# Kernel tuning notes

Measured on AMD Instinct MI355X. Metric: run time of the kernel, lower is better.

## Reference

```python
import jax, jax.numpy as jnp
import numpy as np

PATCH = 9  # patch_size (search window 9x9, i.e. displacement radius 4)


def setup_inputs() -> dict:
    key = jax.random.key(0)
    k1, k2 = jax.random.split(key)
    input1 = jax.random.normal(k1, (8, 128, 96, 128), dtype=jnp.float32)
    input2 = jax.random.normal(k2, (8, 128, 96, 128), dtype=jnp.float32)
    return {"input1": input1, "input2": input2}


def _correlation(input1, input2):
    # kernel_size=1, stride=1, padding=0, dilation=1, dilation_patch=1
    b, c, h, w = input1.shape
    pad_lo = (PATCH - 1) // 2
    pad_hi = PATCH // 2
    p2 = jnp.pad(input2, ((0, 0), (0, 0), (pad_lo, pad_hi), (pad_lo, pad_hi)))

    offs = jnp.arange(PATCH)
    ii, jj = jnp.meshgrid(offs, offs, indexing="ij")
    shifts = jnp.stack([ii.ravel(), jj.ravel()], axis=-1)  # (PATCH*PATCH, 2)

    def one_shift(off):
        win = jax.lax.dynamic_slice(p2, (0, 0, off[0], off[1]), (b, c, h, w))
        # channel-wise dot product at every spatial location
        return jnp.einsum("bchw,bchw->bhw", input1, win)

    corr = jax.vmap(one_shift)(shifts)          # (PATCH*PATCH, b, h, w)
    corr = corr.reshape(PATCH, PATCH, b, h, w)
    return corr.transpose(2, 0, 1, 3, 4)        # (b, PATCH, PATCH, h, w)


def reference(input1, input2):
    return _correlation(input1, input2)
```

## Files before the change

### kernel.cpp

```cpp
#include <hip/hip_runtime.h>

#define HH 96
#define WW 128
#define PP 9
#define RAD 4
#define YT 2
#define CCH 8
#define NCHUNK 16
#define TDI 3
#define ROWS2 (YT + TDI - 1)
#define WB 64
#define HALO (WB + 2 * RAD)
#define GS2 73
#define GS1 65
#define NPAIR2 (ROWS2 * (HALO / 2))
#define NPAIR1 (YT * (WB / 2))
#define NT 192
#define CHS (HH * WW)
#define CSTEP (CCH * CHS)

typedef __fp16 h2v __attribute__((ext_vector_type(2)));
union HU { unsigned int u; h2v h; };

__device__ __forceinline__ unsigned int pk(float a, float b) {
    HU r; r.h = __builtin_amdgcn_cvt_pkrtz(a, b); return r.u;
}
__device__ __forceinline__ float dot2(unsigned int a, unsigned int b, float c) {
    HU ua, ub; ua.u = a; ub.u = b;
    return __builtin_amdgcn_fdot2(ua.h, ub.h, c, false);
}
__device__ __forceinline__ int swz(int g) { return g ^ ((g >> 3) & 7); }

__global__ __launch_bounds__(NT, 6)
void corr_kernel(const float* __restrict__ in1, const float* __restrict__ in2,
                 float* __restrict__ out)
{
    __shared__ uint4 s2[2][ROWS2 * GS2];
    __shared__ uint4 s1[2][YT * GS1];

    const int tid = threadIdx.x;
    const int by  = blockIdx.x >> 1;
    const int bx  = blockIdx.x & 1;
    const int y0  = by * YT;
    const int x0b = bx * WB;
    const int b   = blockIdx.y;
    const int dib = blockIdx.z * TDI;

    const int di3 = tid >> 6;
    const int yl  = (tid >> 5) & 1;
    const int xg  = tid & 31;
    const int x0l = 2 * xg;

    const float* b1 = in1 + (size_t)b * 128 * CHS;
    const float* b2 = in2 + (size_t)b * 128 * CHS;

    const float* tp0; int dA0, dB0; bool tv0, t0is2;
    if (tid < NPAIR2) {
        const int row = tid / 36;
        const int pp  = tid - row * 36;
        const int gy  = y0 - RAD + dib + row;
        const int gx  = x0b + 2 * pp - RAD;
        t0is2 = true;
        tv0   = ((unsigned)gy < HH) && ((unsigned)gx < WW);
        tp0   = b2 + (gy * WW + gx);
        dA0   = row * GS2 + swz(2 * pp);
        dB0   = row * GS2 + swz(2 * pp + 1);
    } else {
        const int u   = tid - NPAIR2;
        const int row = u >> 5;
        const int pp  = u & 31;
        t0is2 = false;
        tv0   = true;
        tp0   = b1 + ((y0 + row) * WW + x0b + 2 * pp);
        dA0   = row * GS1 + swz(2 * pp);
        dB0   = row * GS1 + swz(2 * pp + 1);
    }
    const bool act1 = (tid < 16);
    const float* tp1 = b1 + ((y0 + 1) * WW + x0b + 2 * (16 + tid));
    const int dA1 = GS1 + swz(2 * (16 + tid));
    const int dB1 = GS1 + swz(2 * (16 + tid) + 1);

    float acc[PP][2];
    #pragma unroll
    for (int j = 0; j < PP; ++j) { acc[j][0] = 0.f; acc[j][1] = 0.f; }

    for (int cc = 0; cc < NCHUNK; ++cc) {
        const int buf = cc & 1;
        const int co  = cc * CSTEP;

        {
            float2 f[8];
            #pragma unroll
            for (int j = 0; j < 8; ++j)
                f[j] = tv0 ? *reinterpret_cast<const float2*>(tp0 + co + j * CHS)
                           : make_float2(0.f, 0.f);
            uint4 gA, gB;
            gA.x = pk(f[0].x, f[1].x); gA.y = pk(f[2].x, f[3].x);
            gA.z = pk(f[4].x, f[5].x); gA.w = pk(f[6].x, f[7].x);
            gB.x = pk(f[0].y, f[1].y); gB.y = pk(f[2].y, f[3].y);
            gB.z = pk(f[4].y, f[5].y); gB.w = pk(f[6].y, f[7].y);
            if (t0is2) { s2[buf][dA0] = gA; s2[buf][dB0] = gB; }
            else       { s1[buf][dA0] = gA; s1[buf][dB0] = gB; }
        }
        if (act1) {
            float2 f[8];
            #pragma unroll
            for (int j = 0; j < 8; ++j)
                f[j] = *reinterpret_cast<const float2*>(tp1 + co + j * CHS);
            uint4 gA, gB;
            gA.x = pk(f[0].x, f[1].x); gA.y = pk(f[2].x, f[3].x);
            gA.z = pk(f[4].x, f[5].x); gA.w = pk(f[6].x, f[7].x);
            gB.x = pk(f[0].y, f[1].y); gB.y = pk(f[2].y, f[3].y);
            gB.z = pk(f[4].y, f[5].y); gB.w = pk(f[6].y, f[7].y);
            s1[buf][dA1] = gA; s1[buf][dB1] = gB;
        }
        __syncthreads();

        {
            const uint4* ar = &s1[buf][yl * GS1];
            const uint4 a0 = ar[swz(x0l)];
            const uint4 a1 = ar[swz(x0l + 1)];
            const uint4* r2 = &s2[buf][(yl + di3) * GS2];
            #pragma unroll
            for (int w = 0; w < PP + 1; ++w) {
                const uint4 v = r2[swz(x0l + w)];
                if (w <= PP - 1) {
                    float t = acc[w][0];
                    t = dot2(v.x, a0.x, t); t = dot2(v.y, a0.y, t);
                    t = dot2(v.z, a0.z, t); t = dot2(v.w, a0.w, t);
                    acc[w][0] = t;
                }
                if (w >= 1) {
                    float t = acc[w - 1][1];
                    t = dot2(v.x, a1.x, t); t = dot2(v.y, a1.y, t);
                    t = dot2(v.z, a1.z, t); t = dot2(v.w, a1.w, t);
                    acc[w - 1][1] = t;
                }
            }
        }
    }

    const int y  = y0 + yl;
    const int di = dib + di3;
    const int xo = x0b + x0l;
    #pragma unroll
    for (int dj = 0; dj < PP; ++dj) {
        float* op = out + ((((size_t)(b * PP + di)) * PP + dj) * HH + y) * WW + xo;
        *reinterpret_cast<float2*>(op) = make_float2(acc[dj][0], acc[dj][1]);
    }
}

extern "C" void kernel_launch(void* const* d_in, const int* in_sizes, int n_in,
                              void* d_out, int out_size, void* d_ws, size_t ws_size,
                              hipStream_t stream) {
    const float* in1 = (const float*)d_in[0];
    const float* in2 = (const float*)d_in[1];
    float* out = (float*)d_out;
    dim3 grid((HH / YT) * 2, 8, 3);
    dim3 block(NT);
    corr_kernel<<<grid, block, 0, stream>>>(in1, in2, out);
}
```

Measured before the change: 180.3 us.

## Cover all nine row displacements per block to share input tiles

Removes the grid z-split over row-displacement groups. Each block now has 576 threads and covers all 9 row displacements, so it stages a 10-row halo of input2 and the input1 rows once instead of three times across blocks. This cuts redundant global loads and fp16 packing of input1 and the overlapping input2 rows. In exchange the grid has a third as many blocks, each block is larger, and shared memory per block grows, which may lower occupancy or leave compute units less evenly loaded.

```diff
diff --git a/kernel.cpp b/kernel.cpp
--- a/kernel.cpp
+++ b/kernel.cpp
@@ -7,15 +7,15 @@
 #define YT 2
 #define CCH 8
 #define NCHUNK 16
-#define TDI 3
-#define ROWS2 (YT + TDI - 1)
+#define ROWS2 (YT + PP - 1)
 #define WB 64
 #define HALO (WB + 2 * RAD)
 #define GS2 73
 #define GS1 65
-#define NPAIR2 (ROWS2 * (HALO / 2))
-#define NPAIR1 (YT * (WB / 2))
-#define NT 192
+#define NP2 (ROWS2 * (HALO / 2))
+#define NP1 (YT * (WB / 2))
+#define NTASK (NP2 + NP1)
+#define NT 576
 #define CHS (HH * WW)
 #define CSTEP (CCH * CHS)
 
@@ -31,7 +31,7 @@
 }
 __device__ __forceinline__ int swz(int g) { return g ^ ((g >> 3) & 7); }
 
-__global__ __launch_bounds__(NT, 6)
+__global__ __launch_bounds__(NT, 7)
 void corr_kernel(const float* __restrict__ in1, const float* __restrict__ in2,
                  float* __restrict__ out)
 {
@@ -44,9 +44,8 @@
     const int y0  = by * YT;
     const int x0b = bx * WB;
     const int b   = blockIdx.y;
-    const int dib = blockIdx.z * TDI;
 
-    const int di3 = tid >> 6;
+    const int di  = tid >> 6;
     const int yl  = (tid >> 5) & 1;
     const int xg  = tid & 31;
     const int x0l = 2 * xg;
@@ -54,31 +53,27 @@
     const float* b1 = in1 + (size_t)b * 128 * CHS;
     const float* b2 = in2 + (size_t)b * 128 * CHS;
 
-    const float* tp0; int dA0, dB0; bool tv0, t0is2;
-    if (tid < NPAIR2) {
-        const int row = tid / 36;
-        const int pp  = tid - row * 36;
-        const int gy  = y0 - RAD + dib + row;
-        const int gx  = x0b + 2 * pp - RAD;
-        t0is2 = true;
-        tv0   = ((unsigned)gy < HH) && ((unsigned)gx < WW);
-        tp0   = b2 + (gy * WW + gx);
-        dA0   = row * GS2 + swz(2 * pp);
-        dB0   = row * GS2 + swz(2 * pp + 1);
-    } else {
-        const int u   = tid - NPAIR2;
-        const int row = u >> 5;
-        const int pp  = u & 31;
-        t0is2 = false;
-        tv0   = true;
-        tp0   = b1 + ((y0 + row) * WW + x0b + 2 * pp);
-        dA0   = row * GS1 + swz(2 * pp);
-        dB0   = row * GS1 + swz(2 * pp + 1);
+    const bool act = (tid < NTASK);
+    const float* tp = b1; int dA = 0, dB = 0; bool tv = false, is2 = false;
+    if (tid < NP2) {
+        const int r  = tid / 36;
+        const int p  = tid - r * 36;
+        const int gy = y0 - RAD + r;
+        const int gx = x0b + 2 * p - RAD;
+        is2 = true;
+        tv  = ((unsigned)gy < HH) && ((unsigned)gx < WW);
+        tp  = b2 + (gy * WW + gx);
+        dA  = r * GS2 + swz(2 * p);
+        dB  = r * GS2 + swz(2 * p + 1);
+    } else if (act) {
+        const int u = tid - NP2;
+        const int r = u >> 5;
+        const int p = u & 31;
+        tv  = true;
+        tp  = b1 + ((y0 + r) * WW + x0b + 2 * p);
+        dA  = r * GS1 + swz(2 * p);
+        dB  = r * GS1 + swz(2 * p + 1);
     }
-    const bool act1 = (tid < 16);
-    const float* tp1 = b1 + ((y0 + 1) * WW + x0b + 2 * (16 + tid));
-    const int dA1 = GS1 + swz(2 * (16 + tid));
-    const int dB1 = GS1 + swz(2 * (16 + tid) + 1);
 
     float acc[PP][2];
     #pragma unroll
@@ -88,31 +83,19 @@
         const int buf = cc & 1;
         const int co  = cc * CSTEP;
 
-        {
+        if (act) {
             float2 f[8];
             #pragma unroll
             for (int j = 0; j < 8; ++j)
-                f[j] = tv0 ? *reinterpret_cast<const float2*>(tp0 + co + j * CHS)
-                           : make_float2(0.f, 0.f);
+                f[j] = tv ? *reinterpret_cast<const float2*>(tp + co + j * CHS)
+                          : make_float2(0.f, 0.f);
             uint4 gA, gB;
             gA.x = pk(f[0].x, f[1].x); gA.y = pk(f[2].x, f[3].x);
             gA.z = pk(f[4].x, f[5].x); gA.w = pk(f[6].x, f[7].x);
             gB.x = pk(f[0].y, f[1].y); gB.y = pk(f[2].y, f[3].y);
             gB.z = pk(f[4].y, f[5].y); gB.w = pk(f[6].y, f[7].y);
-            if (t0is2) { s2[buf][dA0] = gA; s2[buf][dB0] = gB; }
-            else       { s1[buf][dA0] = gA; s1[buf][dB0] = gB; }
-        }
-        if (act1) {
-            float2 f[8];
-            #pragma unroll
-            for (int j = 0; j < 8; ++j)
-                f[j] = *reinterpret_cast<const float2*>(tp1 + co + j * CHS);
-            uint4 gA, gB;
-            gA.x = pk(f[0].x, f[1].x); gA.y = pk(f[2].x, f[3].x);
-            gA.z = pk(f[4].x, f[5].x); gA.w = pk(f[6].x, f[7].x);
-            gB.x = pk(f[0].y, f[1].y); gB.y = pk(f[2].y, f[3].y);
-            gB.z = pk(f[4].y, f[5].y); gB.w = pk(f[6].y, f[7].y);
-            s1[buf][dA1] = gA; s1[buf][dB1] = gB;
+            if (is2) { s2[buf][dA] = gA; s2[buf][dB] = gB; }
+            else     { s1[buf][dA] = gA; s1[buf][dB] = gB; }
         }
         __syncthreads();
 
@@ -120,7 +103,7 @@
             const uint4* ar = &s1[buf][yl * GS1];
             const uint4 a0 = ar[swz(x0l)];
             const uint4 a1 = ar[swz(x0l + 1)];
-            const uint4* r2 = &s2[buf][(yl + di3) * GS2];
+            const uint4* r2 = &s2[buf][(yl + di) * GS2];
             #pragma unroll
             for (int w = 0; w < PP + 1; ++w) {
                 const uint4 v = r2[swz(x0l + w)];
@@ -141,7 +124,6 @@
     }
 
     const int y  = y0 + yl;
-    const int di = dib + di3;
     const int xo = x0b + x0l;
     #pragma unroll
     for (int dj = 0; dj < PP; ++dj) {
@@ -156,7 +138,7 @@
     const float* in1 = (const float*)d_in[0];
     const float* in2 = (const float*)d_in[1];
     float* out = (float*)d_out;
-    dim3 grid((HH / YT) * 2, 8, 3);
+    dim3 grid((HH / YT) * 2, 8);
     dim3 block(NT);
     corr_kernel<<<grid, block, 0, stream>>>(in1, in2, out);
 }
```

Measured after the change: 168.6 us. -6.5%, faster.
